# Optimization experiments

Measured on AMD Instinct MI355X. Metric: run time of the kernel, lower is better.

Reference implementation:

```python
import jax, jax.numpy as jnp
import numpy as np

N_NODES = 100000
N_EDGES = 1600000
F_IN = 128
N_GRAPHS = 1000
NUM_CLASSES = 2


def setup_inputs() -> dict:
    key = jax.random.key(0)
    ks = jax.random.split(key, 12)
    x = jax.random.normal(ks[0], (N_NODES, F_IN), jnp.float32)
    edge_index = jax.random.randint(ks[1], (2, N_EDGES), 0, N_NODES, dtype=jnp.int32)
    edge_weight = jnp.ones((N_EDGES,), jnp.float32)
    node_graph_index = jnp.sort(
        jax.random.randint(ks[2], (N_NODES,), 0, N_GRAPHS, dtype=jnp.int32))
    s = 0.05
    params = {
        'W0': jax.random.normal(ks[3], (F_IN, 64), jnp.float32) * s,
        'b0': jnp.zeros((64,), jnp.float32),
        'W1': jax.random.normal(ks[4], (64, 32), jnp.float32) * s,
        'b1': jnp.zeros((32,), jnp.float32),
        'Wm1': jax.random.normal(ks[5], (32, 128), jnp.float32) * s,
        'bm1': jnp.zeros((128,), jnp.float32),
        'Wm2': jax.random.normal(ks[6], (128, NUM_CLASSES), jnp.float32) * s,
        'bm2': jnp.zeros((NUM_CLASSES,), jnp.float32),
    }
    return dict(x=x, edge_index=edge_index, edge_weight=edge_weight,
                node_graph_index=node_graph_index, **params)


def _gcn_norm(edge_index, edge_weight, n_nodes):
    # renormalization trick: add self-loops, D^-1/2 (A+I) D^-1/2
    loop = jnp.arange(n_nodes, dtype=edge_index.dtype)
    src = jnp.concatenate([edge_index[0], loop])
    dst = jnp.concatenate([edge_index[1], loop])
    w = jnp.concatenate([edge_weight, jnp.ones((n_nodes,), edge_weight.dtype)])
    deg = jax.ops.segment_sum(w, dst, num_segments=n_nodes)
    dinv = jnp.where(deg > 0, jax.lax.rsqrt(jnp.maximum(deg, 1e-12)), 0.0)
    norm_w = dinv[src] * w * dinv[dst]
    return src, dst, norm_w


def _gcn_layer(h, src, dst, norm_w, W, b, n_nodes):
    m = h @ W                                # [N, out] dense transform first
    msg = m[src] * norm_w[:, None]           # [E+N, out] irregular gather
    agg = jax.ops.segment_sum(msg, dst, num_segments=n_nodes)
    return jax.nn.relu(agg + b)


def reference(x, edge_index, edge_weight, node_graph_index,
              W0, b0, W1, b1, Wm1, bm1, Wm2, bm2):
    n_nodes = x.shape[0]
    src, dst, norm_w = _gcn_norm(edge_index, edge_weight, n_nodes)
    h = _gcn_layer(x, src, dst, norm_w, W0, b0, n_nodes)   # GCN 64 + relu
    # dropout is identity at inference (training=False default)
    h = _gcn_layer(h, src, dst, norm_w, W1, b1, n_nodes)   # GCN 32 + relu
    g = jax.ops.segment_sum(h, node_graph_index, num_segments=N_GRAPHS)  # sum_pool
    g = jax.nn.relu(g @ Wm1 + bm1)
    logits = g @ Wm2 + bm2
    return logits
```

## Files before the change

kernel.cpp:

```cpp
#include <hip/hip_runtime.h>
#include <hip/hip_bf16.h>

#define F_IN 128
#define NPB 256
#define NPB_SH 8
#define MAXB 512
#define CHUNK 4096
#define CAP 5120

typedef __attribute__((ext_vector_type(8))) short short8;
typedef __attribute__((ext_vector_type(4))) float f32x4;


__device__ __forceinline__ float bf2f(unsigned short u) {
    return __uint_as_float(((unsigned int)u) << 16);
}
__device__ __forceinline__ unsigned short f2bf(float f) {
    unsigned int x = __float_as_uint(f);
    x += 0x7FFFu + ((x >> 16) & 1u);
    return (unsigned short)(x >> 16);
}
__device__ __forceinline__ void bf8_fma(float w, uint4 r, float* a) {
    a[0] = fmaf(w, __uint_as_float(r.x << 16), a[0]);
    a[1] = fmaf(w, __uint_as_float(r.x & 0xFFFF0000u), a[1]);
    a[2] = fmaf(w, __uint_as_float(r.y << 16), a[2]);
    a[3] = fmaf(w, __uint_as_float(r.y & 0xFFFF0000u), a[3]);
    a[4] = fmaf(w, __uint_as_float(r.z << 16), a[4]);
    a[5] = fmaf(w, __uint_as_float(r.z & 0xFFFF0000u), a[5]);
    a[6] = fmaf(w, __uint_as_float(r.w << 16), a[6]);
    a[7] = fmaf(w, __uint_as_float(r.w & 0xFFFF0000u), a[7]);
}

__global__ __launch_bounds__(256) void prep_w_kernel(
    const float* __restrict__ W0, const float* __restrict__ W1,
    unsigned short* __restrict__ W0t, unsigned short* __restrict__ W1t) {
    int t = blockIdx.x * 256 + threadIdx.x;
    int stride = gridDim.x * 256;
    for (int o = t; o < 64 * 128; o += stride) {
        int n = o >> 7, k = o & 127;
        W0t[o] = f2bf(W0[k * 64 + n]);
    }
    for (int o = t; o < 32 * 64; o += stride) {
        int n = o >> 6, k = o & 63;
        W1t[o] = f2bf(W1[k * 32 + n]);
    }
}

__global__ __launch_bounds__(1024) void bucket_fused_kernel(
    const int* __restrict__ src, const int* __restrict__ dst,
    const float* __restrict__ ew, int* __restrict__ gcursor,
    int2* __restrict__ tmp, int E, int nbucket) {
    __shared__ int hist[MAXB];
    __shared__ int gbase[MAXB];
    const int tid = threadIdx.x;
    const int e0 = blockIdx.x * CHUNK;
    const int e1 = min(e0 + CHUNK, E);
    for (int b = tid; b < nbucket; b += 1024) hist[b] = 0;
    __syncthreads();
    for (int e = e0 + tid; e < e1; e += 1024)
        atomicAdd(&hist[dst[e] >> NPB_SH], 1);
    __syncthreads();
    for (int b = tid; b < nbucket; b += 1024) {
        int h = hist[b];
        gbase[b] = (h > 0) ? atomicAdd(&gcursor[b], h) : 0;
        hist[b] = 0;
    }
    __syncthreads();
    for (int e = e0 + tid; e < e1; e += 1024) {
        int d = dst[e];
        int b = d >> NPB_SH;
        int r = atomicAdd(&hist[b], 1);
        tmp[(size_t)b * CAP + gbase[b] + r] =
            make_int2(src[e] | ((d & (NPB - 1)) << 17), __float_as_int(ew[e]));
    }
}

__global__ __launch_bounds__(1024) void csr_kernel(
    const int2* __restrict__ tmp, const int* __restrict__ gcursor,
    int2* __restrict__ es, int* __restrict__ rstart, int* __restrict__ rend,
    float* __restrict__ dinv, int N) {
    __shared__ int cnt[256];
    __shared__ float dw[256];
    __shared__ int off[256];
    __shared__ int cur[256];
    const int t = threadIdx.x;
    const int n0 = blockIdx.x << NPB_SH;
    const size_t seg = (size_t)blockIdx.x * CAP;
    if (t < 256) {
        cnt[t] = 0;
        dw[t] = 0.f;
    }
    __syncthreads();
    const int count = gcursor[blockIdx.x];
    for (int p = t; p < count; p += 1024) {
        int2 e = tmp[seg + p];
        int d = e.x >> 17;
        atomicAdd(&cnt[d], 1);
        atomicAdd(&dw[d], __int_as_float(e.y));
    }
    __syncthreads();
    if (t < 256) off[t] = cnt[t];
    __syncthreads();
    for (int o = 1; o < 256; o <<= 1) {
        int x = 0;
        if (t >= o && t < 256) x = off[t - o];
        __syncthreads();
        if (t < 256) off[t] += x;
        __syncthreads();
    }
    if (t < 256) {
        int v = cnt[t];
        int excl = off[t] - v;
        cur[t] = excl;
        int n = n0 + t;
        if (n < N) {
            rstart[n] = (int)seg + excl;
            rend[n] = (int)seg + excl + v;
            dinv[n] = rsqrtf(fmaxf(1.f + dw[t], 1e-12f));
        }
    }
    __syncthreads();
    for (int p = t; p < count; p += 1024) {
        int2 e = tmp[seg + p];
        int d = e.x >> 17;
        int r = atomicAdd(&cur[d], 1);
        es[seg + r] = make_int2(e.x & 0x1FFFF, e.y);
    }
}

__global__ __launch_bounds__(256) void gemm1_mfma_kernel(
    const float* __restrict__ X, const unsigned short* __restrict__ W0t,
    const float* __restrict__ dinv, unsigned short* __restrict__ M, int N) {
    __shared__ unsigned short Bs[64][136];
    const int tid = threadIdx.x;
    for (int i = tid; i < 64 * 32; i += 256) {
        int n = i >> 5, k4 = i & 31;
        ushort4 v = ((const ushort4*)W0t)[i];
        *(ushort4*)&Bs[n][k4 * 4] = v;
    }
    __syncthreads();
    const int wave = tid >> 6, lane = tid & 63;
    const int m = lane & 15, q = lane >> 4;
    const int rowA = blockIdx.x * 64 + wave * 16 + m;
    const bool rok = rowA < N;
    const float* xrow = X + (size_t)rowA * 128;
    f32x4 acc[4] = {};
#pragma unroll
    for (int ks = 0; ks < 4; ++ks) {
        int k0 = ks * 32 + q * 8;
        float4 u0 = make_float4(0.f, 0.f, 0.f, 0.f);
        float4 u1 = make_float4(0.f, 0.f, 0.f, 0.f);
        if (rok) {
            u0 = *(const float4*)(xrow + k0);
            u1 = *(const float4*)(xrow + k0 + 4);
        }
        short8 a;
        a[0] = (short)f2bf(u0.x); a[1] = (short)f2bf(u0.y);
        a[2] = (short)f2bf(u0.z); a[3] = (short)f2bf(u0.w);
        a[4] = (short)f2bf(u1.x); a[5] = (short)f2bf(u1.y);
        a[6] = (short)f2bf(u1.z); a[7] = (short)f2bf(u1.w);
#pragma unroll
        for (int ct = 0; ct < 4; ++ct) {
            short8 b = *(const short8*)&Bs[ct * 16 + m][k0];
            acc[ct] = __builtin_amdgcn_mfma_f32_16x16x32_bf16(a, b, acc[ct], 0, 0, 0);
        }
    }
#pragma unroll
    for (int r = 0; r < 4; ++r) {
        int crow = blockIdx.x * 64 + wave * 16 + q * 4 + r;
        if (crow < N) {
            float d = dinv[crow];
#pragma unroll
            for (int ct = 0; ct < 4; ++ct)
                M[(size_t)crow * 64 + ct * 16 + m] = f2bf(acc[ct][r] * d);
        }
    }
}

__global__ __launch_bounds__(256) void gemm2_mfma_kernel(
    const unsigned short* __restrict__ H1, const unsigned short* __restrict__ W1t,
    const float* __restrict__ dinv, unsigned short* __restrict__ M, int N) {
    __shared__ unsigned short Bs[32][72];
    const int tid = threadIdx.x;
    for (int i = tid; i < 32 * 16; i += 256) {
        int n = i >> 4, k4 = i & 15;
        ushort4 v = ((const ushort4*)W1t)[i];
        *(ushort4*)&Bs[n][k4 * 4] = v;
    }
    __syncthreads();
    const int wave = tid >> 6, lane = tid & 63;
    const int m = lane & 15, q = lane >> 4;
    const int rowA = blockIdx.x * 64 + wave * 16 + m;
    const bool rok = rowA < N;
    const short8 az = {0, 0, 0, 0, 0, 0, 0, 0};
    f32x4 acc[2] = {};
#pragma unroll
    for (int ks = 0; ks < 2; ++ks) {
        int k0 = ks * 32 + q * 8;
        short8 a = rok ? *(const short8*)(H1 + (size_t)rowA * 64 + k0) : az;
#pragma unroll
        for (int ct = 0; ct < 2; ++ct) {
            short8 b = *(const short8*)&Bs[ct * 16 + m][k0];
            acc[ct] = __builtin_amdgcn_mfma_f32_16x16x32_bf16(a, b, acc[ct], 0, 0, 0);
        }
    }
#pragma unroll
    for (int r = 0; r < 4; ++r) {
        int crow = blockIdx.x * 64 + wave * 16 + q * 4 + r;
        if (crow < N) {
            float d = dinv[crow];
#pragma unroll
            for (int ct = 0; ct < 2; ++ct)
                M[(size_t)crow * 32 + ct * 16 + m] = f2bf(acc[ct][r] * d);
        }
    }
}

__global__ __launch_bounds__(256) void pull1_kernel(
    const int* __restrict__ rstart, const int* __restrict__ rend,
    const int2* __restrict__ es, const unsigned short* __restrict__ M,
    const float* __restrict__ dinv, const float* __restrict__ bias,
    unsigned short* __restrict__ H1, int N) {
    const int lane = threadIdx.x & 63;
    const int wave = threadIdx.x >> 6;
    const int nd = lane >> 5;
    const int node = blockIdx.x * 8 + wave * 2 + nd;
    if (node >= N) return;
    const int c = lane & 7;
    const int q = (lane >> 3) & 3;
    float acc[8] = {0.f, 0.f, 0.f, 0.f, 0.f, 0.f, 0.f, 0.f};
    if (q == 0) {
        uint4 r = *(const uint4*)(M + (size_t)node * 64 + c * 8);
        bf8_fma(1.f, r, acc);
    }
    const int b = rstart[node], e = rend[node];
    int p = b + q;
    const int e4 = e - 4;
    for (; p < e4; p += 8) {
        int2 ed0 = es[p];
        int2 ed1 = es[p + 4];
        uint4 r0 = *(const uint4*)(M + (size_t)ed0.x * 64 + c * 8);
        uint4 r1 = *(const uint4*)(M + (size_t)ed1.x * 64 + c * 8);
        bf8_fma(__int_as_float(ed0.y), r0, acc);
        bf8_fma(__int_as_float(ed1.y), r1, acc);
    }
    if (p < e) {
        int2 ed = es[p];
        uint4 r = *(const uint4*)(M + (size_t)ed.x * 64 + c * 8);
        bf8_fma(__int_as_float(ed.y), r, acc);
    }
#pragma unroll
    for (int off = 8; off <= 16; off <<= 1)
#pragma unroll
        for (int k = 0; k < 8; ++k) acc[k] += __shfl_xor(acc[k], off);
    if (q == 0) {
        float d = dinv[node];
        const float* bp = bias + c * 8;
        float4 b0v = *(const float4*)(bp);
        float4 b1v = *(const float4*)(bp + 4);
        unsigned short o[8];
        o[0] = f2bf(fmaxf(fmaf(d, acc[0], b0v.x), 0.f));
        o[1] = f2bf(fmaxf(fmaf(d, acc[1], b0v.y), 0.f));
        o[2] = f2bf(fmaxf(fmaf(d, acc[2], b0v.z), 0.f));
        o[3] = f2bf(fmaxf(fmaf(d, acc[3], b0v.w), 0.f));
        o[4] = f2bf(fmaxf(fmaf(d, acc[4], b1v.x), 0.f));
        o[5] = f2bf(fmaxf(fmaf(d, acc[5], b1v.y), 0.f));
        o[6] = f2bf(fmaxf(fmaf(d, acc[6], b1v.z), 0.f));
        o[7] = f2bf(fmaxf(fmaf(d, acc[7], b1v.w), 0.f));
        uint4 pk;
        pk.x = (unsigned int)o[0] | ((unsigned int)o[1] << 16);
        pk.y = (unsigned int)o[2] | ((unsigned int)o[3] << 16);
        pk.z = (unsigned int)o[4] | ((unsigned int)o[5] << 16);
        pk.w = (unsigned int)o[6] | ((unsigned int)o[7] << 16);
        *(uint4*)(H1 + (size_t)node * 64 + c * 8) = pk;
    }
}

__global__ __launch_bounds__(256) void pull2_pool_kernel(
    const int* __restrict__ rstart, const int* __restrict__ rend,
    const int2* __restrict__ es, const unsigned short* __restrict__ M,
    const float* __restrict__ dinv, const float* __restrict__ bias,
    const int* __restrict__ ngi, float* __restrict__ g, int N) {
    __shared__ float4 sh[16][8];
    __shared__ int sgx[16];
    const int t = threadIdx.x;
    const int lane = t & 63;
    const int nl = t >> 4;
    const int node = blockIdx.x * 16 + nl;
    const int c = lane & 3;
    const int q = (lane >> 2) & 3;
    const bool valid = node < N;
    float acc[8] = {0.f, 0.f, 0.f, 0.f, 0.f, 0.f, 0.f, 0.f};
    if (valid) {
        if (q == 0) {
            uint4 r = *(const uint4*)(M + (size_t)node * 32 + c * 8);
            bf8_fma(1.f, r, acc);
        }
        const int b = rstart[node], e = rend[node];
        int p = b + q;
        const int e4 = e - 4;
        for (; p < e4; p += 8) {
            int2 ed0 = es[p];
            int2 ed1 = es[p + 4];
            uint4 r0 = *(const uint4*)(M + (size_t)ed0.x * 32 + c * 8);
            uint4 r1 = *(const uint4*)(M + (size_t)ed1.x * 32 + c * 8);
            bf8_fma(__int_as_float(ed0.y), r0, acc);
            bf8_fma(__int_as_float(ed1.y), r1, acc);
        }
        if (p < e) {
            int2 ed = es[p];
            uint4 r = *(const uint4*)(M + (size_t)ed.x * 32 + c * 8);
            bf8_fma(__int_as_float(ed.y), r, acc);
        }
#pragma unroll
        for (int off = 4; off <= 8; off <<= 1)
#pragma unroll
            for (int k = 0; k < 8; ++k) acc[k] += __shfl_xor(acc[k], off);
    }
    if (q == 0) {
        float4 o0 = make_float4(0.f, 0.f, 0.f, 0.f);
        float4 o1 = make_float4(0.f, 0.f, 0.f, 0.f);
        if (valid) {
            float d = dinv[node];
            const float* bp = bias + c * 8;
            float4 b0v = *(const float4*)(bp);
            float4 b1v = *(const float4*)(bp + 4);
            o0.x = fmaxf(fmaf(d, acc[0], b0v.x), 0.f);
            o0.y = fmaxf(fmaf(d, acc[1], b0v.y), 0.f);
            o0.z = fmaxf(fmaf(d, acc[2], b0v.z), 0.f);
            o0.w = fmaxf(fmaf(d, acc[3], b0v.w), 0.f);
            o1.x = fmaxf(fmaf(d, acc[4], b1v.x), 0.f);
            o1.y = fmaxf(fmaf(d, acc[5], b1v.y), 0.f);
            o1.z = fmaxf(fmaf(d, acc[6], b1v.z), 0.f);
            o1.w = fmaxf(fmaf(d, acc[7], b1v.w), 0.f);
        }
        sh[nl][c * 2] = o0;
        sh[nl][c * 2 + 1] = o1;
        if (c == 0) sgx[nl] = valid ? ngi[node] : -1;
    }
    __syncthreads();
    if (t < 8) {
        int cc = t;
        float4 a = make_float4(0.f, 0.f, 0.f, 0.f);
        int cg = -1;
        for (int i = 0; i < 16; ++i) {
            int gi = sgx[i];
            if (gi < 0) continue;
            if (gi != cg) {
                if (cg >= 0) {
                    float* gp = g + cg * 32 + cc * 4;
                    atomicAdd(gp + 0, a.x); atomicAdd(gp + 1, a.y);
                    atomicAdd(gp + 2, a.z); atomicAdd(gp + 3, a.w);
                }
                cg = gi;
                a = sh[i][cc];
            } else {
                float4 tv = sh[i][cc];
                a.x += tv.x; a.y += tv.y; a.z += tv.z; a.w += tv.w;
            }
        }
        if (cg >= 0) {
            float* gp = g + cg * 32 + cc * 4;
            atomicAdd(gp + 0, a.x); atomicAdd(gp + 1, a.y);
            atomicAdd(gp + 2, a.z); atomicAdd(gp + 3, a.w);
        }
    }
}

__global__ __launch_bounds__(128) void mlp_kernel(
    const float* __restrict__ g, const float* __restrict__ Wm1,
    const float* __restrict__ bm1, const float* __restrict__ Wm2,
    const float* __restrict__ bm2, float* __restrict__ out) {
    __shared__ float sg[32];
    __shared__ float st[128];
    int b = blockIdx.x, t = threadIdx.x;
    if (t < 32) sg[t] = g[b * 32 + t];
    __syncthreads();
    float acc = bm1[t];
#pragma unroll
    for (int k = 0; k < 32; ++k) acc = fmaf(sg[k], Wm1[k * 128 + t], acc);
    st[t] = fmaxf(acc, 0.f);
    __syncthreads();
    if (t < 2) {
        float o = bm2[t];
#pragma unroll
        for (int k = 0; k < 128; ++k) o = fmaf(st[k], Wm2[k * 2 + t], o);
        out[b * 2 + t] = o;
    }
}


extern "C" void kernel_launch(void* const* d_in, const int* in_sizes, int n_in,
                              void* d_out, int out_size, void* d_ws, size_t ws_size,
                              hipStream_t stream) {
    const float* x   = (const float*)d_in[0];
    const int*   ei  = (const int*)d_in[1];
    const float* ew  = (const float*)d_in[2];
    const int*   ngi = (const int*)d_in[3];
    const float* W0  = (const float*)d_in[4];
    const float* b0  = (const float*)d_in[5];
    const float* W1  = (const float*)d_in[6];
    const float* b1  = (const float*)d_in[7];
    const float* Wm1 = (const float*)d_in[8];
    const float* bm1 = (const float*)d_in[9];
    const float* Wm2 = (const float*)d_in[10];
    const float* bm2 = (const float*)d_in[11];
    float* out = (float*)d_out;

    const int N = in_sizes[0] / F_IN;
    const int E = in_sizes[1] / 2;
    const int G = out_size / 2;
    const int* srcp = ei;
    const int* dstp = ei + E;
    const int NBUCKET = (N + NPB - 1) >> NPB_SH;
    const int NBLK = (E + CHUNK - 1) / CHUNK;

    char* wsb = (char*)d_ws;
    size_t off = 0;
    auto alloc = [&](size_t bytes) {
        char* p = wsb + off;
        off += (bytes + 255) & ~(size_t)255;
        return p;
    };
    float* dinv     = (float*)alloc((size_t)N * 4);
    int*   gcursor  = (int*)  alloc((size_t)NBUCKET * 4);
    int*   rstart   = (int*)  alloc((size_t)N * 4);
    int*   rend     = (int*)  alloc((size_t)N * 4);
    int2*  tmp      = (int2*) alloc((size_t)NBUCKET * CAP * 8);
    int2*  es       = (int2*) alloc((size_t)NBUCKET * CAP * 8);
    unsigned short* W0t = (unsigned short*)alloc(64 * 128 * 2);
    unsigned short* W1t = (unsigned short*)alloc(32 * 64 * 2);
    unsigned short* M   = (unsigned short*)alloc((size_t)N * 64 * 2);
    unsigned short* H1  = (unsigned short*)alloc((size_t)N * 64 * 2);
    float* Gbuf     = (float*)alloc((size_t)G * 32 * 4);
    unsigned short* m1p = M;

    hipMemsetAsync(gcursor, 0, (size_t)NBUCKET * 4, stream);
    prep_w_kernel<<<8, 256, 0, stream>>>(W0, W1, W0t, W1t);
    bucket_fused_kernel<<<NBLK, 1024, 0, stream>>>(srcp, dstp, ew, gcursor, tmp, E, NBUCKET);
    csr_kernel<<<NBUCKET, 1024, 0, stream>>>(tmp, gcursor, es, rstart, rend, dinv, N);

    gemm1_mfma_kernel<<<(N + 63) / 64, 256, 0, stream>>>(x, W0t, dinv, M, N);
    pull1_kernel<<<(N + 7) / 8, 256, 0, stream>>>(rstart, rend, es, M, dinv, b0, H1, N);

    gemm2_mfma_kernel<<<(N + 63) / 64, 256, 0, stream>>>(H1, W1t, dinv, m1p, N);
    hipMemsetAsync(Gbuf, 0, (size_t)G * 32 * 4, stream);
    pull2_pool_kernel<<<(N + 15) / 16, 256, 0, stream>>>(rstart, rend, es, m1p, dinv, b1, ngi, Gbuf, N);

    mlp_kernel<<<G, 128, 0, stream>>>(Gbuf, Wm1, bm1, Wm2, bm2, out);
}
```

Before: 244.5 us.

## Vectorize edge loads, fold memsets into prep kernel, shuffle-reduce MLP output

The two memsets are folded into the weight-prep kernel, which removes two separate operations from the stream. The bucket and CSR kernels now read dst/src/weights and the temporary edge pairs with 128-bit loads instead of one element at a time. The pull kernels give each quarter-group a contiguous slice of a node's edge list and read two edges at once with an int4 load, cutting the number of load instructions for edge metadata. The MLP's final 128x2 product becomes a wavefront shuffle reduction instead of a serial loop in two threads. The int4 loads on the edge list can start at 8-byte rather than 16-byte aligned addresses, and the contiguous slices change how edge reads coalesce across lanes.

```diff
diff --git a/kernel.cpp b/kernel.cpp
--- a/kernel.cpp
+++ b/kernel.cpp
@@ -33,7 +33,9 @@
 
 __global__ __launch_bounds__(256) void prep_w_kernel(
     const float* __restrict__ W0, const float* __restrict__ W1,
-    unsigned short* __restrict__ W0t, unsigned short* __restrict__ W1t) {
+    unsigned short* __restrict__ W0t, unsigned short* __restrict__ W1t,
+    int* __restrict__ gcursor, float* __restrict__ Gbuf,
+    int nbucket, int gtot) {
     int t = blockIdx.x * 256 + threadIdx.x;
     int stride = gridDim.x * 256;
     for (int o = t; o < 64 * 128; o += stride) {
@@ -44,6 +46,8 @@
         int n = o >> 6, k = o & 63;
         W1t[o] = f2bf(W1[k * 32 + n]);
     }
+    for (int o = t; o < nbucket; o += stride) gcursor[o] = 0;
+    for (int o = t; o < gtot; o += stride) Gbuf[o] = 0.f;
 }
 
 __global__ __launch_bounds__(1024) void bucket_fused_kernel(
@@ -57,8 +61,23 @@
     const int e1 = min(e0 + CHUNK, E);
     for (int b = tid; b < nbucket; b += 1024) hist[b] = 0;
     __syncthreads();
-    for (int e = e0 + tid; e < e1; e += 1024)
-        atomicAdd(&hist[dst[e] >> NPB_SH], 1);
+    const int e = e0 + (tid << 2);
+    const bool vec = (e + 4 <= e1);
+    const int nsc = vec ? 0 : max(0, e1 - e);
+    int4 d4 = make_int4(0, 0, 0, 0);
+    if (vec) {
+        d4 = *(const int4*)(dst + e);
+        atomicAdd(&hist[d4.x >> NPB_SH], 1);
+        atomicAdd(&hist[d4.y >> NPB_SH], 1);
+        atomicAdd(&hist[d4.z >> NPB_SH], 1);
+        atomicAdd(&hist[d4.w >> NPB_SH], 1);
+    } else {
+        for (int j = 0; j < nsc; ++j) {
+            int d = dst[e + j];
+            ((int*)&d4)[j] = d;
+            atomicAdd(&hist[d >> NPB_SH], 1);
+        }
+    }
     __syncthreads();
     for (int b = tid; b < nbucket; b += 1024) {
         int h = hist[b];
@@ -66,12 +85,41 @@
         hist[b] = 0;
     }
     __syncthreads();
-    for (int e = e0 + tid; e < e1; e += 1024) {
-        int d = dst[e];
-        int b = d >> NPB_SH;
-        int r = atomicAdd(&hist[b], 1);
-        tmp[(size_t)b * CAP + gbase[b] + r] =
-            make_int2(src[e] | ((d & (NPB - 1)) << 17), __float_as_int(ew[e]));
+    if (vec) {
+        int4 s4 = *(const int4*)(src + e);
+        float4 w4 = *(const float4*)(ew + e);
+        {
+            int d = d4.x, b = d >> NPB_SH;
+            int r = atomicAdd(&hist[b], 1);
+            tmp[(size_t)b * CAP + gbase[b] + r] =
+                make_int2(s4.x | ((d & (NPB - 1)) << 17), __float_as_int(w4.x));
+        }
+        {
+            int d = d4.y, b = d >> NPB_SH;
+            int r = atomicAdd(&hist[b], 1);
+            tmp[(size_t)b * CAP + gbase[b] + r] =
+                make_int2(s4.y | ((d & (NPB - 1)) << 17), __float_as_int(w4.y));
+        }
+        {
+            int d = d4.z, b = d >> NPB_SH;
+            int r = atomicAdd(&hist[b], 1);
+            tmp[(size_t)b * CAP + gbase[b] + r] =
+                make_int2(s4.z | ((d & (NPB - 1)) << 17), __float_as_int(w4.z));
+        }
+        {
+            int d = d4.w, b = d >> NPB_SH;
+            int r = atomicAdd(&hist[b], 1);
+            tmp[(size_t)b * CAP + gbase[b] + r] =
+                make_int2(s4.w | ((d & (NPB - 1)) << 17), __float_as_int(w4.w));
+        }
+    } else {
+        for (int j = 0; j < nsc; ++j) {
+            int d = ((int*)&d4)[j];
+            int b = d >> NPB_SH;
+            int r = atomicAdd(&hist[b], 1);
+            tmp[(size_t)b * CAP + gbase[b] + r] =
+                make_int2(src[e + j] | ((d & (NPB - 1)) << 17), __float_as_int(ew[e + j]));
+        }
     }
 }
 
@@ -92,11 +140,20 @@
     }
     __syncthreads();
     const int count = gcursor[blockIdx.x];
-    for (int p = t; p < count; p += 1024) {
-        int2 e = tmp[seg + p];
-        int d = e.x >> 17;
+    const int pairs = count >> 1;
+    for (int i = t; i < pairs; i += 1024) {
+        int4 v = *(const int4*)(tmp + seg + 2 * i);
+        int d0 = v.x >> 17, d1 = v.z >> 17;
+        atomicAdd(&cnt[d0], 1);
+        atomicAdd(&dw[d0], __int_as_float(v.y));
+        atomicAdd(&cnt[d1], 1);
+        atomicAdd(&dw[d1], __int_as_float(v.w));
+    }
+    if ((count & 1) && t == 0) {
+        int2 e2 = tmp[seg + count - 1];
+        int d = e2.x >> 17;
         atomicAdd(&cnt[d], 1);
-        atomicAdd(&dw[d], __int_as_float(e.y));
+        atomicAdd(&dw[d], __int_as_float(e2.y));
     }
     __syncthreads();
     if (t < 256) off[t] = cnt[t];
@@ -120,11 +177,19 @@
         }
     }
     __syncthreads();
-    for (int p = t; p < count; p += 1024) {
-        int2 e = tmp[seg + p];
-        int d = e.x >> 17;
+    for (int i = t; i < pairs; i += 1024) {
+        int4 v = *(const int4*)(tmp + seg + 2 * i);
+        int d0 = v.x >> 17, d1 = v.z >> 17;
+        int r0 = atomicAdd(&cur[d0], 1);
+        es[seg + r0] = make_int2(v.x & 0x1FFFF, v.y);
+        int r1 = atomicAdd(&cur[d1], 1);
+        es[seg + r1] = make_int2(v.z & 0x1FFFF, v.w);
+    }
+    if ((count & 1) && t == 0) {
+        int2 e2 = tmp[seg + count - 1];
+        int d = e2.x >> 17;
         int r = atomicAdd(&cur[d], 1);
-        es[seg + r] = make_int2(e.x & 0x1FFFF, e.y);
+        es[seg + r] = make_int2(e2.x & 0x1FFFF, e2.y);
     }
 }
 
@@ -234,17 +299,18 @@
         bf8_fma(1.f, r, acc);
     }
     const int b = rstart[node], e = rend[node];
-    int p = b + q;
-    const int e4 = e - 4;
-    for (; p < e4; p += 8) {
-        int2 ed0 = es[p];
-        int2 ed1 = es[p + 4];
-        uint4 r0 = *(const uint4*)(M + (size_t)ed0.x * 64 + c * 8);
-        uint4 r1 = *(const uint4*)(M + (size_t)ed1.x * 64 + c * 8);
-        bf8_fma(__int_as_float(ed0.y), r0, acc);
-        bf8_fma(__int_as_float(ed1.y), r1, acc);
-    }
-    if (p < e) {
+    const int len = e - b;
+    const int base = len >> 2, rem = len & 3;
+    int p = b + q * base + min(q, rem);
+    const int pe = p + base + (q < rem ? 1 : 0);
+    for (; p + 2 <= pe; p += 2) {
+        int4 v = *(const int4*)(es + p);
+        uint4 r0 = *(const uint4*)(M + (size_t)v.x * 64 + c * 8);
+        uint4 r1 = *(const uint4*)(M + (size_t)v.z * 64 + c * 8);
+        bf8_fma(__int_as_float(v.y), r0, acc);
+        bf8_fma(__int_as_float(v.w), r1, acc);
+    }
+    if (p < pe) {
         int2 ed = es[p];
         uint4 r = *(const uint4*)(M + (size_t)ed.x * 64 + c * 8);
         bf8_fma(__int_as_float(ed.y), r, acc);
@@ -297,17 +363,18 @@
             bf8_fma(1.f, r, acc);
         }
         const int b = rstart[node], e = rend[node];
-        int p = b + q;
-        const int e4 = e - 4;
-        for (; p < e4; p += 8) {
-            int2 ed0 = es[p];
-            int2 ed1 = es[p + 4];
-            uint4 r0 = *(const uint4*)(M + (size_t)ed0.x * 32 + c * 8);
-            uint4 r1 = *(const uint4*)(M + (size_t)ed1.x * 32 + c * 8);
-            bf8_fma(__int_as_float(ed0.y), r0, acc);
-            bf8_fma(__int_as_float(ed1.y), r1, acc);
-        }
-        if (p < e) {
+        const int len = e - b;
+        const int base = len >> 2, rem = len & 3;
+        int p = b + q * base + min(q, rem);
+        const int pe = p + base + (q < rem ? 1 : 0);
+        for (; p + 2 <= pe; p += 2) {
+            int4 v = *(const int4*)(es + p);
+            uint4 r0 = *(const uint4*)(M + (size_t)v.x * 32 + c * 8);
+            uint4 r1 = *(const uint4*)(M + (size_t)v.z * 32 + c * 8);
+            bf8_fma(__int_as_float(v.y), r0, acc);
+            bf8_fma(__int_as_float(v.w), r1, acc);
+        }
+        if (p < pe) {
             int2 ed = es[p];
             uint4 r = *(const uint4*)(M + (size_t)ed.x * 32 + c * 8);
             bf8_fma(__int_as_float(ed.y), r, acc);
@@ -372,21 +439,27 @@
     const float* __restrict__ bm1, const float* __restrict__ Wm2,
     const float* __restrict__ bm2, float* __restrict__ out) {
     __shared__ float sg[32];
-    __shared__ float st[128];
+    __shared__ float red[4];
     int b = blockIdx.x, t = threadIdx.x;
     if (t < 32) sg[t] = g[b * 32 + t];
     __syncthreads();
     float acc = bm1[t];
 #pragma unroll
     for (int k = 0; k < 32; ++k) acc = fmaf(sg[k], Wm1[k * 128 + t], acc);
-    st[t] = fmaxf(acc, 0.f);
-    __syncthreads();
-    if (t < 2) {
-        float o = bm2[t];
-#pragma unroll
-        for (int k = 0; k < 128; ++k) o = fmaf(st[k], Wm2[k * 2 + t], o);
-        out[b * 2 + t] = o;
-    }
+    float h = fmaxf(acc, 0.f);
+    float p0 = h * Wm2[t * 2 + 0];
+    float p1 = h * Wm2[t * 2 + 1];
+#pragma unroll
+    for (int off = 32; off >= 1; off >>= 1) {
+        p0 += __shfl_xor(p0, off);
+        p1 += __shfl_xor(p1, off);
+    }
+    if ((t & 63) == 0) {
+        red[(t >> 6) * 2 + 0] = p0;
+        red[(t >> 6) * 2 + 1] = p1;
+    }
+    __syncthreads();
+    if (t < 2) out[b * 2 + t] = bm2[t] + red[t] + red[2 + t];
 }
 
 
@@ -435,8 +508,7 @@
     float* Gbuf     = (float*)alloc((size_t)G * 32 * 4);
     unsigned short* m1p = M;
 
-    hipMemsetAsync(gcursor, 0, (size_t)NBUCKET * 4, stream);
-    prep_w_kernel<<<8, 256, 0, stream>>>(W0, W1, W0t, W1t);
+    prep_w_kernel<<<8, 256, 0, stream>>>(W0, W1, W0t, W1t, gcursor, Gbuf, NBUCKET, G * 32);
     bucket_fused_kernel<<<NBLK, 1024, 0, stream>>>(srcp, dstp, ew, gcursor, tmp, E, NBUCKET);
     csr_kernel<<<NBUCKET, 1024, 0, stream>>>(tmp, gcursor, es, rstart, rend, dinv, N);
 
@@ -444,7 +516,6 @@
     pull1_kernel<<<(N + 7) / 8, 256, 0, stream>>>(rstart, rend, es, M, dinv, b0, H1, N);
 
     gemm2_mfma_kernel<<<(N + 63) / 64, 256, 0, stream>>>(H1, W1t, dinv, m1p, N);
-    hipMemsetAsync(Gbuf, 0, (size_t)G * 32 * 4, stream);
     pull2_pool_kernel<<<(N + 15) / 16, 256, 0, stream>>>(rstart, rend, es, m1p, dinv, b1, ngi, Gbuf, N);
 
     mlp_kernel<<<G, 128, 0, stream>>>(Gbuf, Wm1, bm1, Wm2, bm2, out);
```

After: 240.2 us. Within noise of the previous version (-1.7%).
